# Optimization experiments

Hardware: AMD Instinct MI355X
Metric: run time of the kernel (lower is better)

The kernel has to match this reference:

```python
import jax, jax.numpy as jnp
import numpy as np
import math

B, N, D, S = 128, 2048, 512, 64  # batch, nodes, d_model, state_features


def setup_inputs() -> dict:
    key = jax.random.key(0)
    k1, k2, k3, k4, k5 = jax.random.split(key, 5)
    node_embeddings = jax.random.normal(k1, (B, N, D), dtype=jnp.float32)
    truck_state = jax.random.normal(k2, (B, S), dtype=jnp.float32)
    mask = jax.random.bernoulli(k3, 0.3, (B, N))  # True = masked-out node
    Wq = jax.random.normal(k4, (D, S), dtype=jnp.float32) * 0.05  # query_proj weight
    bq = jnp.zeros((D,), dtype=jnp.float32)
    Ws = jax.random.normal(k5, (D, D), dtype=jnp.float32) * 0.02  # scores_proj weight
    bs = jnp.zeros((D,), dtype=jnp.float32)
    return {"node_embeddings": node_embeddings, "truck_state": truck_state,
            "mask": mask, "Wq": Wq, "bq": bq, "Ws": Ws, "bs": bs}


def reference(node_embeddings, truck_state, mask, Wq, bq, Ws, bs):
    d_model = node_embeddings.shape[-1]
    scale = 1.0 / math.sqrt(d_model)
    # query = query_proj(truck_state): [B, D]
    query = truck_state @ Wq.T + bq
    # single-query attention scores over nodes: [B, N]
    attn_scores = jnp.einsum('bd,bnd->bn', query, node_embeddings) * scale
    attn_scores = jnp.where(mask, -jnp.inf, attn_scores)
    attn_weights = jax.nn.softmax(attn_scores, axis=-1)
    # context: [B, D]
    context = jnp.einsum('bn,bnd->bd', attn_weights, node_embeddings)
    # scores = scores_proj(context): [B, D]
    scores = context @ Ws.T + bs
    # dot-product logits per node: [B, N]
    logits = jnp.einsum('bnd,bd->bn', node_embeddings, scores) * scale
    logits = jnp.where(mask, -jnp.inf, logits)
    return logits
```

## Files before the change

kernel.cpp:

```cpp
#include <hip/hip_runtime.h>
#include <math.h>

#define BB 128
#define NN 2048
#define DD 512
#define SS 64
#define NCH 16
#define CH (NN / NCH)
#define NPW (CH / 8)
#define SCALE 0.044194173824159216f
#define NEG_BIG (-1.0e30f)

__device__ __forceinline__ float dot8(float4 a0, float4 a1, float4 b0, float4 b1) {
    return a0.x*b0.x + a0.y*b0.y + a0.z*b0.z + a0.w*b0.w
         + a1.x*b1.x + a1.y*b1.y + a1.z*b1.z + a1.w*b1.w;
}

__global__ __launch_bounds__(512, 8) void k_pass1(
    const float* __restrict__ node, const unsigned char* __restrict__ mask,
    const float* __restrict__ ts, const float* __restrict__ Wq,
    const float* __restrict__ bq,
    float* __restrict__ part_ctx, float* __restrict__ part_m,
    float* __restrict__ part_l)
{
    int bid   = blockIdx.x;
    int b     = bid >> 4;
    int chunk = bid & 15;
    int wave  = threadIdx.x >> 6;
    int lane  = threadIdx.x & 63;
    int dbase = lane * 8;

    __shared__ float q_lds[DD];
    __shared__ float lds_ctx[8][DD];
    __shared__ float lds_m[8], lds_l[8];

    {
        int d = threadIdx.x;
        const float4* tv = (const float4*)(ts + b * SS);
        const float4* wv = (const float4*)(Wq + (size_t)d * SS);
        float acc = 0.f;
#pragma unroll
        for (int k = 0; k < SS / 4; ++k) {
            float4 a = tv[k], w = wv[k];
            acc += a.x*w.x + a.y*w.y + a.z*w.z + a.w*w.w;
        }
        q_lds[d] = acc + bq[d];
    }

    int n0 = chunk * CH + wave * NPW;
    const unsigned char* mrow = mask + (size_t)b * NN;
    unsigned long long bal = __ballot(mrow[n0 + (lane & 15)] == 0);
    unsigned int live = (unsigned int)(bal & 0xffffull);
    __syncthreads();

    float4 q0 = *(const float4*)&q_lds[dbase];
    float4 q1 = *(const float4*)&q_lds[dbase + 4];

    float m = NEG_BIG, l = 0.f;
    float c0=0,c1=0,c2=0,c3=0,c4=0,c5=0,c6=0,c7=0;
    const float* rp = node + ((size_t)b * NN + n0) * DD + dbase;

#pragma unroll 1
    for (int j = 0; j < NPW; j += 2) {
        float4 v0a = *(const float4*)rp;
        float4 v0b = *(const float4*)(rp + 4);
        const float* rp1 = rp + DD;
        float4 v1a = *(const float4*)rp1;
        float4 v1b = *(const float4*)(rp1 + 4);
        rp += 2 * DD;
        float dp0 = dot8(q0, q1, v0a, v0b);
        float dp1 = dot8(q0, q1, v1a, v1b);
#pragma unroll
        for (int off = 32; off; off >>= 1) {
            dp0 += __shfl_xor(dp0, off, 64);
            dp1 += __shfl_xor(dp1, off, 64);
        }
        bool a0 = (live >> j) & 1u;
        bool a1 = (live >> (j + 1)) & 1u;
        float s0 = a0 ? dp0 * SCALE : NEG_BIG;
        float s1 = a1 ? dp1 * SCALE : NEG_BIG;
        float nm = fmaxf(m, fmaxf(s0, s1));
        float r  = __expf(m - nm);
        float p0 = a0 ? __expf(s0 - nm) : 0.f;
        float p1 = a1 ? __expf(s1 - nm) : 0.f;
        l = l * r + p0 + p1;
        c0 = c0*r + p0*v0a.x + p1*v1a.x;
        c1 = c1*r + p0*v0a.y + p1*v1a.y;
        c2 = c2*r + p0*v0a.z + p1*v1a.z;
        c3 = c3*r + p0*v0a.w + p1*v1a.w;
        c4 = c4*r + p0*v0b.x + p1*v1b.x;
        c5 = c5*r + p0*v0b.y + p1*v1b.y;
        c6 = c6*r + p0*v0b.z + p1*v1b.z;
        c7 = c7*r + p0*v0b.w + p1*v1b.w;
        m = nm;
    }

    if (lane == 0) { lds_m[wave] = m; lds_l[wave] = l; }
    __syncthreads();
    float M = lds_m[0];
#pragma unroll
    for (int w = 1; w < 8; ++w) M = fmaxf(M, lds_m[w]);
    float f = __expf(m - M);
    *(float4*)&lds_ctx[wave][dbase]     = make_float4(c0*f, c1*f, c2*f, c3*f);
    *(float4*)&lds_ctx[wave][dbase + 4] = make_float4(c4*f, c5*f, c6*f, c7*f);
    __syncthreads();
    {
        int d = threadIdx.x;
        float acc = 0.f;
#pragma unroll
        for (int w = 0; w < 8; ++w) acc += lds_ctx[w][d];
        part_ctx[(size_t)bid * DD + d] = acc;
    }
    if (threadIdx.x == 0) {
        float L = 0.f;
#pragma unroll
        for (int w = 0; w < 8; ++w) L += __expf(lds_m[w] - M) * lds_l[w];
        part_m[bid] = M;
        part_l[bid] = L;
    }
}

__global__ __launch_bounds__(256) void k_scores(
    const float* __restrict__ part_ctx, const float* __restrict__ part_m,
    const float* __restrict__ part_l,
    const float* __restrict__ Ws, const float* __restrict__ bs,
    float* __restrict__ scores)
{
    int b    = blockIdx.x >> 2;
    int qt   = blockIdx.x & 3;
    int wave = threadIdx.x >> 6;
    int lane = threadIdx.x & 63;
    int dbase = lane * 8;
    __shared__ float ctx[DD];

    float M = NEG_BIG;
#pragma unroll
    for (int c = 0; c < NCH; ++c) M = fmaxf(M, part_m[(b << 4) | c]);
    float L = 0.f;
    float fc[NCH];
#pragma unroll
    for (int c = 0; c < NCH; ++c) {
        fc[c] = __expf(part_m[(b << 4) | c] - M);
        L += fc[c] * part_l[(b << 4) | c];
    }
    float Linv = 1.f / fmaxf(L, 1e-30f);

    for (int d = threadIdx.x; d < DD; d += 256) {
        float acc = 0.f;
#pragma unroll
        for (int c = 0; c < NCH; ++c)
            acc += fc[c] * part_ctx[(size_t)((b << 4) | c) * DD + d];
        ctx[d] = acc * Linv;
    }
    __syncthreads();

    float4 x0 = *(const float4*)&ctx[dbase];
    float4 x1 = *(const float4*)&ctx[dbase + 4];
    for (int j = 0; j < 32; ++j) {
        int dd = qt * 128 + wave * 32 + j;
        const float* wrow = Ws + (size_t)dd * DD + dbase;
        float4 w0 = *(const float4*)wrow;
        float4 w1 = *(const float4*)(wrow + 4);
        float dp = dot8(x0, x1, w0, w1);
#pragma unroll
        for (int off = 32; off; off >>= 1) dp += __shfl_xor(dp, off, 64);
        if (lane == 0) scores[b * DD + dd] = dp + bs[dd];
    }
}

__global__ __launch_bounds__(256, 8) void k_logits(
    const float* __restrict__ node, const unsigned char* __restrict__ mask,
    const float* __restrict__ scores, float* __restrict__ out)
{
    int wave = threadIdx.x >> 6;
    int lane = threadIdx.x & 63;
    int dbase = lane * 8;
    int wg = blockIdx.x * 4 + wave;
    int rg = 32767 - wg;
    int g0 = rg * 8;
    int b  = g0 >> 11;

    unsigned long long mb = *(const unsigned long long*)(mask + g0);

    const float* sc = scores + b * DD + dbase;
    float4 t0 = *(const float4*)sc;
    float4 t1 = *(const float4*)(sc + 4);

#pragma unroll 1
    for (int i = 7; i >= 0; --i) {
        int g = g0 + i;
        if ((mb >> (8 * i)) & 0xffull) {
            if (lane == 0) out[g] = NEG_BIG;
            continue;
        }
        const float* rp = node + (size_t)g * DD + dbase;
        float4 va = *(const float4*)rp;
        float4 vb = *(const float4*)(rp + 4);
        float dp = dot8(t0, t1, va, vb);
#pragma unroll
        for (int off = 32; off; off >>= 1) dp += __shfl_xor(dp, off, 64);
        if (lane == 0) out[g] = dp * SCALE;
    }
}

extern "C" void kernel_launch(void* const* d_in, const int* in_sizes, int n_in,
                              void* d_out, int out_size, void* d_ws, size_t ws_size,
                              hipStream_t stream)
{
    const float*         node = (const float*)d_in[0];
    const float*         ts   = (const float*)d_in[1];
    const unsigned char* mask = (const unsigned char*)d_in[2];
    const float*         Wq   = (const float*)d_in[3];
    const float*         bq   = (const float*)d_in[4];
    const float*         Ws   = (const float*)d_in[5];
    const float*         bs   = (const float*)d_in[6];
    float* out = (float*)d_out;

    float* ws       = (float*)d_ws;
    float* part_ctx = ws;
    float* part_m   = part_ctx + BB * NCH * DD;
    float* part_l   = part_m + BB * NCH;
    float* scores   = part_l + BB * NCH;

    k_pass1 <<<BB * NCH, 512, 0, stream>>>(node, mask, ts, Wq, bq,
                                           part_ctx, part_m, part_l);
    k_scores<<<BB * 4, 256, 0, stream>>>(part_ctx, part_m, part_l, Ws, bs, scores);
    k_logits<<<(BB * NN) / 32, 256, 0, stream>>>(node, mask, scores, out);
}
```

Baseline: 209.5 us.

## Skip loading masked node rows and hoist query projection into its own kernel

```diff
diff --git a/kernel.cpp b/kernel.cpp
--- a/kernel.cpp
+++ b/kernel.cpp
@@ -16,10 +16,26 @@
          + a1.x*b1.x + a1.y*b1.y + a1.z*b1.z + a1.w*b1.w;
 }
 
+__global__ __launch_bounds__(512) void k_query(
+    const float* __restrict__ ts, const float* __restrict__ Wq,
+    const float* __restrict__ bq, float* __restrict__ query)
+{
+    int b = blockIdx.x;
+    int d = threadIdx.x;
+    const float4* tv = (const float4*)(ts + b * SS);
+    const float4* wv = (const float4*)(Wq + (size_t)d * SS);
+    float acc = 0.f;
+#pragma unroll
+    for (int k = 0; k < SS / 4; ++k) {
+        float4 a = tv[k], w = wv[k];
+        acc += a.x*w.x + a.y*w.y + a.z*w.z + a.w*w.w;
+    }
+    query[b * DD + d] = acc + bq[d];
+}
+
 __global__ __launch_bounds__(512, 8) void k_pass1(
     const float* __restrict__ node, const unsigned char* __restrict__ mask,
-    const float* __restrict__ ts, const float* __restrict__ Wq,
-    const float* __restrict__ bq,
+    const float* __restrict__ query,
     float* __restrict__ part_ctx, float* __restrict__ part_m,
     float* __restrict__ part_l)
 {
@@ -30,44 +46,30 @@
     int lane  = threadIdx.x & 63;
     int dbase = lane * 8;
 
-    __shared__ float q_lds[DD];
     __shared__ float lds_ctx[8][DD];
     __shared__ float lds_m[8], lds_l[8];
 
-    {
-        int d = threadIdx.x;
-        const float4* tv = (const float4*)(ts + b * SS);
-        const float4* wv = (const float4*)(Wq + (size_t)d * SS);
-        float acc = 0.f;
-#pragma unroll
-        for (int k = 0; k < SS / 4; ++k) {
-            float4 a = tv[k], w = wv[k];
-            acc += a.x*w.x + a.y*w.y + a.z*w.z + a.w*w.w;
-        }
-        q_lds[d] = acc + bq[d];
-    }
+    float4 q0 = *(const float4*)(query + b * DD + dbase);
+    float4 q1 = *(const float4*)(query + b * DD + dbase + 4);
 
     int n0 = chunk * CH + wave * NPW;
     const unsigned char* mrow = mask + (size_t)b * NN;
     unsigned long long bal = __ballot(mrow[n0 + (lane & 15)] == 0);
-    unsigned int live = (unsigned int)(bal & 0xffffull);
-    __syncthreads();
-
-    float4 q0 = *(const float4*)&q_lds[dbase];
-    float4 q1 = *(const float4*)&q_lds[dbase + 4];
+    unsigned int lv = (unsigned int)(bal & 0xffffull);
 
     float m = NEG_BIG, l = 0.f;
     float c0=0,c1=0,c2=0,c3=0,c4=0,c5=0,c6=0,c7=0;
-    const float* rp = node + ((size_t)b * NN + n0) * DD + dbase;
-
-#pragma unroll 1
-    for (int j = 0; j < NPW; j += 2) {
-        float4 v0a = *(const float4*)rp;
-        float4 v0b = *(const float4*)(rp + 4);
-        const float* rp1 = rp + DD;
-        float4 v1a = *(const float4*)rp1;
-        float4 v1b = *(const float4*)(rp1 + 4);
-        rp += 2 * DD;
+    const float* basep = node + ((size_t)b * NN + n0) * DD + dbase;
+
+    while (lv) {
+        int j0 = __ffs(lv) - 1; lv &= lv - 1;
+        bool has2 = (lv != 0);
+        int j1 = has2 ? (__ffs(lv) - 1) : j0;
+        lv = has2 ? (lv & (lv - 1)) : lv;
+        const float* r0 = basep + (size_t)j0 * DD;
+        const float* r1 = basep + (size_t)j1 * DD;
+        float4 v0a = *(const float4*)r0, v0b = *(const float4*)(r0 + 4);
+        float4 v1a = *(const float4*)r1, v1b = *(const float4*)(r1 + 4);
         float dp0 = dot8(q0, q1, v0a, v0b);
         float dp1 = dot8(q0, q1, v1a, v1b);
 #pragma unroll
@@ -75,14 +77,12 @@
             dp0 += __shfl_xor(dp0, off, 64);
             dp1 += __shfl_xor(dp1, off, 64);
         }
-        bool a0 = (live >> j) & 1u;
-        bool a1 = (live >> (j + 1)) & 1u;
-        float s0 = a0 ? dp0 * SCALE : NEG_BIG;
-        float s1 = a1 ? dp1 * SCALE : NEG_BIG;
+        float s0 = dp0 * SCALE;
+        float s1 = has2 ? dp1 * SCALE : NEG_BIG;
         float nm = fmaxf(m, fmaxf(s0, s1));
         float r  = __expf(m - nm);
-        float p0 = a0 ? __expf(s0 - nm) : 0.f;
-        float p1 = a1 ? __expf(s1 - nm) : 0.f;
+        float p0 = __expf(s0 - nm);
+        float p1 = has2 ? __expf(s1 - nm) : 0.f;
         l = l * r + p0 + p1;
         c0 = c0*r + p0*v0a.x + p1*v1a.x;
         c1 = c1*r + p0*v0a.y + p1*v1a.y;
@@ -182,24 +182,38 @@
 
     unsigned long long mb = *(const unsigned long long*)(mask + g0);
 
+    if (lane < 8 && ((mb >> (8 * lane)) & 0xffull)) out[g0 + lane] = NEG_BIG;
+
+    unsigned int lv = 0;
+#pragma unroll
+    for (int i = 0; i < 8; ++i)
+        lv |= (((mb >> (8 * i)) & 0xffull) == 0ull ? 1u : 0u) << i;
+
     const float* sc = scores + b * DD + dbase;
     float4 t0 = *(const float4*)sc;
     float4 t1 = *(const float4*)(sc + 4);
-
-#pragma unroll 1
-    for (int i = 7; i >= 0; --i) {
-        int g = g0 + i;
-        if ((mb >> (8 * i)) & 0xffull) {
-            if (lane == 0) out[g] = NEG_BIG;
-            continue;
+    const float* basep = node + (size_t)g0 * DD + dbase;
+
+    while (lv) {
+        int j0 = __ffs(lv) - 1; lv &= lv - 1;
+        bool has2 = (lv != 0);
+        int j1 = has2 ? (__ffs(lv) - 1) : j0;
+        lv = has2 ? (lv & (lv - 1)) : lv;
+        const float* r0 = basep + (size_t)j0 * DD;
+        const float* r1 = basep + (size_t)j1 * DD;
+        float4 v0a = *(const float4*)r0, v0b = *(const float4*)(r0 + 4);
+        float4 v1a = *(const float4*)r1, v1b = *(const float4*)(r1 + 4);
+        float dp0 = dot8(t0, t1, v0a, v0b);
+        float dp1 = dot8(t0, t1, v1a, v1b);
+#pragma unroll
+        for (int off = 32; off; off >>= 1) {
+            dp0 += __shfl_xor(dp0, off, 64);
+            dp1 += __shfl_xor(dp1, off, 64);
         }
-        const float* rp = node + (size_t)g * DD + dbase;
-        float4 va = *(const float4*)rp;
-        float4 vb = *(const float4*)(rp + 4);
-        float dp = dot8(t0, t1, va, vb);
-#pragma unroll
-        for (int off = 32; off; off >>= 1) dp += __shfl_xor(dp, off, 64);
-        if (lane == 0) out[g] = dp * SCALE;
+        if (lane == 0) {
+            out[g0 + j0] = dp0 * SCALE;
+            if (has2) out[g0 + j1] = dp1 * SCALE;
+        }
     }
 }
 
@@ -221,8 +235,10 @@
     float* part_m   = part_ctx + BB * NCH * DD;
     float* part_l   = part_m + BB * NCH;
     float* scores   = part_l + BB * NCH;
-
-    k_pass1 <<<BB * NCH, 512, 0, stream>>>(node, mask, ts, Wq, bq,
+    float* query    = scores + BB * DD;
+
+    k_query <<<BB, 512, 0, stream>>>(ts, Wq, bq, query);
+    k_pass1 <<<BB * NCH, 512, 0, stream>>>(node, mask, query,
                                            part_ctx, part_m, part_l);
     k_scores<<<BB * 4, 256, 0, stream>>>(part_ctx, part_m, part_l, Ws, bs, scores);
     k_logits<<<(BB * NN) / 32, 256, 0, stream>>>(node, mask, scores, out);
```

Measured after the change: 200.7 us. 1.04x faster.
